# Performance work log

Measured on AMD Instinct MI355X. Metric: run time of the kernel, lower is better.

Reference implementation:

```python
import jax, jax.numpy as jnp
import numpy as np
from jax import lax

RATIOS = jnp.array([0.5, 1.0, 2.0], dtype=jnp.float32)
SCALES = jnp.array([8.0, 16.0, 32.0], dtype=jnp.float32)
IOU_THR = 0.5
BATCH_SIZE = 32            # module-level constant in the source
POS_RATIO = 1.0 / 3.0      # positive_ratio in the source


def _generate_anchors(fh, fw, ih, iw):
    """Vectorized version of RPN.generate_anchors. Returns (A,4) x1y1x2y2 anchors
    and an (A,) inside-image mask (static shapes; mask replaces boolean filtering)."""
    xs = iw / fw
    ys = ih / fh
    xc = (jnp.arange(fw, dtype=jnp.float32) + 0.5) * xs
    yc = (jnp.arange(fh, dtype=jnp.float32) + 0.5) * ys
    gx, gy = jnp.meshgrid(xc, yc, indexing='ij')
    centers = jnp.stack([gx.ravel(), gy.ravel()], axis=1)          # (fh*fw, 2)
    h = jnp.sqrt(SCALES[None, :] ** 2 / RATIOS[:, None]) * ys       # (3,3)
    w = h * RATIOS[:, None] * xs / ys
    wh = jnp.stack([w.ravel(), h.ravel()], axis=1)                  # (9, 2)
    lo = centers[:, None, :] - wh[None, :, :] / 2
    hi = centers[:, None, :] + wh[None, :, :] / 2
    anchors = jnp.concatenate([lo, hi], axis=2).reshape(-1, 4)      # (A, 4)
    inside = ((anchors[:, 0] >= 0) & (anchors[:, 1] >= 0) &
              (anchors[:, 2] <= iw) & (anchors[:, 3] <= ih))
    return anchors, inside


def _iou_matrix(anchors, gts):
    """Pairwise IoU between (A,4) and (G,4) corner boxes -> (A,G). Vectorizes the
    nested python loop in the original."""
    x1 = jnp.maximum(anchors[:, None, 0], gts[None, :, 0])
    y1 = jnp.maximum(anchors[:, None, 1], gts[None, :, 1])
    x2 = jnp.minimum(anchors[:, None, 2], gts[None, :, 2])
    y2 = jnp.minimum(anchors[:, None, 3], gts[None, :, 3])
    inter = jnp.maximum(x2 - x1, 0.0) * jnp.maximum(y2 - y1, 0.0)
    area_a = (anchors[:, 2] - anchors[:, 0]) * (anchors[:, 3] - anchors[:, 1])
    area_g = (gts[:, 2] - gts[:, 0]) * (gts[:, 3] - gts[:, 1])
    union = area_a[:, None] + area_g[None, :] - inter
    return jnp.where(inter > 0, inter / union, 0.0)


def _conv(x, w, b):
    return lax.conv_general_dilated(x, w, (1, 1), 'SAME',
                                    dimension_numbers=('NHWC', 'HWIO', 'NHWC')) + b


def setup_inputs() -> dict:
    key = jax.random.key(0)
    ks = jax.random.split(key, 11)
    B, H, W, C = 8, 64, 64, 512
    IMG = 1024
    std = 0.05  # keras RandomNormal default stddev
    features = jax.random.normal(ks[0], (B, H, W, C), jnp.float32)
    # 8 rows of boxes; rows 2..7 are the object boxes used by the RPN (x1,y1,x2,y2)
    xy = jax.random.uniform(ks[1], (8, 2), jnp.float32) * (IMG * 0.7)
    wh = jax.random.uniform(ks[2], (8, 2), jnp.float32) * (IMG * 0.2) + 16.0
    ground_truths = jnp.concatenate([xy, xy + wh], axis=1)
    return {
        'features': features,
        'ground_truths': ground_truths,
        'conv1_w': jax.random.normal(ks[3], (3, 3, C, 512), jnp.float32) * std,
        'conv1_b': jnp.zeros((512,), jnp.float32),
        'reg_w': jax.random.normal(ks[4], (1, 1, 512, 72), jnp.float32) * std,
        'reg_b': jnp.zeros((72,), jnp.float32),
        'cls_w': jax.random.normal(ks[5], (1, 1, 512, 9), jnp.float32) * std,
        'cls_b': jnp.zeros((9,), jnp.float32),
        'lmk_w': jax.random.normal(ks[6], (1, 1, 512, 54), jnp.float32) * std,
        'lmk_b': jnp.zeros((54,), jnp.float32),
        'img_h': IMG,
        'img_w': IMG,
    }


def reference(features, ground_truths, conv1_w, conv1_b, reg_w, reg_b,
              cls_w, cls_b, lmk_w, lmk_b, img_h, img_w):
    B, H, W, C = features.shape
    anchors, inside = _generate_anchors(H, W, float(img_h), float(img_w))
    A = anchors.shape[0]
    gts = ground_truths[2:]                                   # (6,4)
    ious = _iou_matrix(anchors, gts)                          # (A,6)
    ious = jnp.where(inside[:, None], ious, -1.0)             # outside anchors never match

    best_iou = ious.max(axis=1)
    best_idx = ious.argmax(axis=1)
    gt_best = ious.max(axis=0)
    is_best = ((ious == gt_best[None, :]) & (gt_best[None, :] > -1.0)).any(axis=1)
    labels = jnp.where((best_iou >= IOU_THR) | is_best, 1, 0)
    labels = jnp.where(inside, labels, -1)

    # balanced subsampling (np.random.choice in the original -> rank-of-random trick)
    num_pos = int(POS_RATIO * BATCH_SIZE)
    num_neg = BATCH_SIZE - num_pos
    r = jax.random.uniform(jax.random.key(42), (A,), jnp.float32)

    def keep(mask, n):
        kv = jnp.where(mask, r, jnp.inf)
        order = jnp.argsort(kv)
        rank = jnp.zeros(A, jnp.int32).at[order].set(jnp.arange(A, dtype=jnp.int32))
        return mask & (rank < n)

    pos = keep(labels == 1, num_pos)
    neg = keep(labels == 0, num_neg)
    labels = jnp.where(pos, 1, jnp.where(neg, 0, -1)).astype(jnp.float32)

    eps = jnp.finfo(jnp.float32).eps
    wa = jnp.maximum(anchors[:, 2] - anchors[:, 0], eps)
    ha = jnp.maximum(anchors[:, 3] - anchors[:, 1], eps)
    xa = anchors[:, 0] + wa / 2
    ya = anchors[:, 1] + ha / 2
    mg = gts[best_idx]                                        # (A,4) matched gt
    wg = mg[:, 2] - mg[:, 0]
    hg = mg[:, 3] - mg[:, 1]
    xg = mg[:, 0] + wg / 2
    yg = mg[:, 1] + hg / 2
    deltas = jnp.stack([(xg - xa) / wa, (yg - ya) / ha,
                        jnp.log(wg / wa), jnp.log(hg / ha)], axis=1)
    offsets = jnp.where(pos[:, None], deltas, 0.0)            # (A,4)

    # conv heads on backbone features
    x = jax.nn.relu(_conv(features, conv1_w, conv1_b))
    anchor_deltas = _conv(x, reg_w, reg_b)                    # (B,H,W,72)
    scores = jax.nn.sigmoid(_conv(x, cls_w, cls_b))           # (B,H,W,9)
    landmarks = _conv(x, lmk_w, lmk_b)                        # (B,H,W,54)
    return anchor_deltas, scores, landmarks, labels, offsets
```

## Files before the change

kernel.cpp:

```cpp
#include <hip/hip_runtime.h>
#include <cstdint>
#include <cstddef>


#define A_TOT 36864

typedef unsigned short ushortT;
typedef __attribute__((ext_vector_type(8))) short short8;
typedef __attribute__((ext_vector_type(4))) float f32x4;

typedef __attribute__((address_space(1))) unsigned char gbyte_t;
typedef __attribute__((address_space(3))) unsigned char lbyte_t;

__device__ __forceinline__ void gld_lds16(const void* g, void* l) {
  __builtin_amdgcn_global_load_lds((gbyte_t*)g, (lbyte_t*)l, 16, 0, 0);
}

__device__ __forceinline__ uint32_t rotl32(uint32_t v, int d) { return (v << d) | (v >> (32 - d)); }

__device__ __forceinline__ ushortT f2bf(float f) {
  uint32_t u = __float_as_uint(f);
  uint32_t r = (u + 0x7FFFu + ((u >> 16) & 1u)) >> 16;
  return (ushortT)r;
}

__device__ __forceinline__ uint32_t f2mono(float f) {
  uint32_t b = __float_as_uint(f);
  return b ^ ((b >> 31) ? 0xFFFFFFFFu : 0x80000000u);
}
__device__ __forceinline__ float mono2f(uint32_t u) {
  uint32_t b = (u >> 31) ? (u ^ 0x80000000u) : ~u;
  return __uint_as_float(b);
}

__device__ uint32_t threefry_bits_for(uint32_t a) {
  uint32_t x0 = 0u, x1 = a;
  const uint32_t k0 = 0u, k1 = 42u;
  const uint32_t k2 = k0 ^ k1 ^ 0x1BD11BDAu;
  x0 += k0; x1 += k1;
#define TF_RND(r) { x0 += x1; x1 = rotl32(x1, (r)); x1 ^= x0; }
  TF_RND(13) TF_RND(15) TF_RND(26) TF_RND(6)
  x0 += k1; x1 += k2 + 1u;
  TF_RND(17) TF_RND(29) TF_RND(16) TF_RND(24)
  x0 += k2; x1 += k0 + 2u;
  TF_RND(13) TF_RND(15) TF_RND(26) TF_RND(6)
  x0 += k0; x1 += k1 + 3u;
  TF_RND(17) TF_RND(29) TF_RND(16) TF_RND(24)
  x0 += k1; x1 += k2 + 4u;
  TF_RND(13) TF_RND(15) TF_RND(26) TF_RND(6)
  x0 += k2; x1 += k0 + 5u;
#undef TF_RND
  return x0 ^ x1;
}

struct Anc { float x1, y1, x2, y2; bool inside; };

__device__ __forceinline__ Anc anchor_at(int a, float iw, float ih) {
  Anc A;
  {
    #pragma clang fp contract(off)
    int p = a / 9;
    int q = a - p * 9;
    int i = p >> 6;
    int j = p & 63;
    int ri = q / 3;
    int si = q - ri * 3;
    const float ratios[3] = {0.5f, 1.0f, 2.0f};
    const float scales[3] = {8.0f, 16.0f, 32.0f};
    float xs = iw / 64.0f;
    float ys = ih / 64.0f;
    float cx = ((float)i + 0.5f) * xs;
    float cy = ((float)j + 0.5f) * ys;
    float r = ratios[ri], s = scales[si];
    float h = sqrtf((s * s) / r) * ys;
    float w = h * r * xs / ys;
    A.x1 = cx - w * 0.5f;
    A.y1 = cy - h * 0.5f;
    A.x2 = cx + w * 0.5f;
    A.y2 = cy + h * 0.5f;
    A.inside = (A.x1 >= 0.0f) && (A.y1 >= 0.0f) && (A.x2 <= iw) && (A.y2 <= ih);
  }
  return A;
}

__device__ __forceinline__ float iou_one(const Anc& A, const float* g) {
  #pragma clang fp contract(off)
  float x1 = fmaxf(A.x1, g[0]);
  float y1 = fmaxf(A.y1, g[1]);
  float x2 = fminf(A.x2, g[2]);
  float y2 = fminf(A.y2, g[3]);
  float inter = fmaxf(x2 - x1, 0.0f) * fmaxf(y2 - y1, 0.0f);
  float area_a = (A.x2 - A.x1) * (A.y2 - A.y1);
  float area_g = (g[2] - g[0]) * (g[3] - g[1]);
  float un = (area_a + area_g) - inter;
  return inter > 0.0f ? (inter / un) : 0.0f;
}

__global__ __launch_bounds__(256) void labels_gtmax_kernel(
    const float* __restrict__ gtr, const int* __restrict__ pih, const int* __restrict__ piw,
    uint32_t* __restrict__ gtbest_bits) {
  __shared__ float s_gt[6][4];
  __shared__ float s_red[4][6];
  int tid = threadIdx.x;
  if (tid < 24) ((float*)s_gt)[tid] = gtr[8 + tid];
  __syncthreads();
  float iw = (float)piw[0], ih = (float)pih[0];
  int a = blockIdx.x * 256 + tid;
  Anc A = anchor_at(a, iw, ih);
  int w = tid >> 6;
  #pragma unroll
  for (int g = 0; g < 6; ++g) {
    float v = A.inside ? iou_one(A, s_gt[g]) : -1.0f;
    for (int off = 32; off > 0; off >>= 1) v = fmaxf(v, __shfl_down(v, off, 64));
    if ((tid & 63) == 0) s_red[w][g] = v;
  }
  __syncthreads();
  if (tid < 6) {
    float m = fmaxf(fmaxf(s_red[0][tid], s_red[1][tid]), fmaxf(s_red[2][tid], s_red[3][tid]));
    atomicMax(&gtbest_bits[tid], f2mono(m));
  }
}

__global__ __launch_bounds__(256) void labels_code_kernel(
    const float* __restrict__ gtr, const int* __restrict__ pih, const int* __restrict__ piw,
    const uint32_t* __restrict__ gtbest_bits, uint32_t* __restrict__ L) {
  __shared__ float s_gt[6][4];
  __shared__ float s_gb[6];
  int tid = threadIdx.x;
  if (tid < 24) ((float*)s_gt)[tid] = gtr[8 + tid];
  if (tid < 6) s_gb[tid] = mono2f(gtbest_bits[tid]);
  __syncthreads();
  float iw = (float)piw[0], ih = (float)pih[0];
  int a = blockIdx.x * 256 + tid;
  Anc A = anchor_at(a, iw, ih);
  uint32_t code;
  if (!A.inside) {
    code = 2u;
  } else {
    float best = -1.0f;
    bool isb = false;
    #pragma unroll
    for (int g = 0; g < 6; ++g) {
      float v = iou_one(A, s_gt[g]);
      best = fmaxf(best, v);
      if (v == s_gb[g] && s_gb[g] > -1.0f) isb = true;
    }
    code = (best >= 0.5f || isb) ? 1u : 0u;
  }
  uint32_t m = threefry_bits_for((uint32_t)a) >> 9;
  L[a] = (m << 2) | code;
}

__global__ __launch_bounds__(1024) void labels_select_kernel(
    const uint32_t* __restrict__ L, unsigned long long* __restrict__ Tsel) {
  __shared__ int hist[2][512];
  __shared__ unsigned long long list[2][512];
  __shared__ int lcnt[2];
  __shared__ int s_b[2], s_r[2];
  int tid = threadIdx.x;
  hist[tid >> 9][tid & 511] = 0;
  if (tid < 2) lcnt[tid] = 0;
  __syncthreads();
  for (int a = tid; a < A_TOT; a += 1024) {
    uint32_t v = L[a];
    uint32_t c = v & 3u;
    if (c < 2u) atomicAdd(&hist[c][v >> 16], 1);
  }
  __syncthreads();
  if (tid < 2) {
    int need = (tid == 1) ? 10 : 22;
    int tot = 0;
    for (int i = 0; i < 512; ++i) tot += hist[tid][i];
    int b = -1, r = 0, cum = 0;
    if (tot > need) {
      for (int i = 0; i < 512; ++i) {
        if (cum + hist[tid][i] >= need) { b = i; r = need - cum; break; }
        cum += hist[tid][i];
      }
    }
    s_b[tid] = b; s_r[tid] = r;
    if (b < 0) Tsel[tid] = ~0ull;
  }
  __syncthreads();
  for (int a = tid; a < A_TOT; a += 1024) {
    uint32_t v = L[a];
    uint32_t c = v & 3u;
    if (c < 2u && s_b[c] == (int)(v >> 16)) {
      int idx = atomicAdd(&lcnt[c], 1);
      if (idx < 512) list[c][idx] = (((unsigned long long)(v >> 2)) << 16) | (unsigned)a;
    }
  }
  __syncthreads();
  #pragma unroll
  for (int c = 0; c < 2; ++c) {
    if (s_b[c] < 0) continue;
    int n = lcnt[c] < 512 ? lcnt[c] : 512;
    if (tid < n) {
      unsigned long long k = list[c][tid];
      int rank = 1;
      for (int i = 0; i < n; ++i) rank += (list[c][i] < k) ? 1 : 0;
      if (rank == s_r[c]) Tsel[c] = k;
    }
  }
}

__global__ __launch_bounds__(256) void labels_final_kernel(
    const uint32_t* __restrict__ L, const unsigned long long* __restrict__ Tsel,
    const float* __restrict__ gtr, const int* __restrict__ pih, const int* __restrict__ piw,
    float* __restrict__ labels_out, float* __restrict__ offs_out) {
  __shared__ float s_gt[6][4];
  int tid = threadIdx.x;
  if (tid < 24) ((float*)s_gt)[tid] = gtr[8 + tid];
  __syncthreads();
  float iw = (float)piw[0], ih = (float)pih[0];
  int a = blockIdx.x * 256 + tid;
  uint32_t v = L[a];
  uint32_t code = v & 3u;
  unsigned long long K = (((unsigned long long)(v >> 2)) << 16) | (unsigned)a;
  bool pos = (code == 1u) && (K <= Tsel[1]);
  bool neg = (code == 0u) && (K <= Tsel[0]);
  labels_out[a] = pos ? 1.0f : (neg ? 0.0f : -1.0f);
  float o0 = 0.0f, o1 = 0.0f, o2 = 0.0f, o3 = 0.0f;
  if (pos) {
    #pragma clang fp contract(off)
    Anc A = anchor_at(a, iw, ih);
    int bi = 0;
    float bv = iou_one(A, s_gt[0]);
    for (int g = 1; g < 6; ++g) {
      float vg = iou_one(A, s_gt[g]);
      if (vg > bv) { bv = vg; bi = g; }
    }
    const float eps = 1.1920928955078125e-07f;
    float wa = fmaxf(A.x2 - A.x1, eps);
    float ha = fmaxf(A.y2 - A.y1, eps);
    float xa = A.x1 + wa * 0.5f;
    float ya = A.y1 + ha * 0.5f;
    const float* g = s_gt[bi];
    float wg = g[2] - g[0];
    float hg = g[3] - g[1];
    float xg = g[0] + wg * 0.5f;
    float yg = g[1] + hg * 0.5f;
    o0 = (xg - xa) / wa;
    o1 = (yg - ya) / ha;
    o2 = logf(wg / wa);
    o3 = logf(hg / ha);
  }
  offs_out[a * 4 + 0] = o0;
  offs_out[a * 4 + 1] = o1;
  offs_out[a * 4 + 2] = o2;
  offs_out[a * 4 + 3] = o3;
}

__global__ __launch_bounds__(256) void prep_wt_kernel(
    const float* __restrict__ w, ushortT* __restrict__ Wt) {
  __shared__ float tile[64][65];
  int blk = blockIdx.x;
  int kk = blk / 64;
  int rem = blk - kk * 64;
  int ic0 = (rem >> 3) * 64;
  int oc0 = (rem & 7) * 64;
  int t = threadIdx.x;
  int tr = t >> 6;
  int tc = t & 63;
  #pragma unroll
  for (int r = 0; r < 16; ++r) {
    int ic = tr * 16 + r;
    tile[ic][tc] = w[((size_t)(kk * 512 + ic0 + ic)) * 512 + oc0 + tc];
  }
  __syncthreads();
  #pragma unroll
  for (int r = 0; r < 16; ++r) {
    int oc = tr * 16 + r;
    Wt[((size_t)(kk * 512 + oc0 + oc)) * 512 + ic0 + tc] = f2bf(tile[tc][oc]);
  }
}

__global__ void prep_misc_kernel(const float* __restrict__ feat,
                                 const float* __restrict__ reg_w, const float* __restrict__ cls_w,
                                 const float* __restrict__ lmk_w, const float* __restrict__ reg_b,
                                 const float* __restrict__ cls_b, const float* __restrict__ lmk_b,
                                 ushortT* __restrict__ featbf, ushortT* __restrict__ zrow,
                                 ushortT* __restrict__ Wh, float* __restrict__ bias_all,
                                 uint32_t* __restrict__ gtbest_bits, int do_feat) {
  int idx = blockIdx.x * 256 + threadIdx.x;
  if (do_feat) {
    const float4 f0 = *(const float4*)(feat + (size_t)idx * 8);
    const float4 f1 = *(const float4*)(feat + (size_t)idx * 8 + 4);
    short8 o;
    o[0] = (short)f2bf(f0.x); o[1] = (short)f2bf(f0.y);
    o[2] = (short)f2bf(f0.z); o[3] = (short)f2bf(f0.w);
    o[4] = (short)f2bf(f1.x); o[5] = (short)f2bf(f1.y);
    o[6] = (short)f2bf(f1.z); o[7] = (short)f2bf(f1.w);
    *(short8*)(featbf + (size_t)idx * 8) = o;
  }
  if (idx < 73728) {
    int c = idx >> 9, ic = idx & 511;
    float v = 0.0f;
    if (c < 72) v = reg_w[ic * 72 + c];
    else if (c < 81) v = cls_w[ic * 9 + (c - 72)];
    else if (c < 135) v = lmk_w[ic * 54 + (c - 81)];
    Wh[idx] = f2bf(v);
  }
  if (do_feat && idx < 4096) {
    *(short8*)(zrow + (size_t)idx * 8) = (short8){0, 0, 0, 0, 0, 0, 0, 0};
  }
  if (idx < 144) {
    float bv = 0.0f;
    if (idx < 72) bv = reg_b[idx];
    else if (idx < 81) bv = cls_b[idx - 72];
    else if (idx < 135) bv = lmk_b[idx - 81];
    bias_all[idx] = bv;
  }
  if (idx < 6) gtbest_bits[idx] = f2mono(-1.0f);
}

__global__ __launch_bounds__(256) void conv3x3_mfma_kernel(
    const ushortT* __restrict__ featbf, const ushortT* __restrict__ zrow,
    const ushortT* __restrict__ Wt, const float* __restrict__ bias,
    ushortT* __restrict__ xbf) {
  __shared__ __align__(16) char smem[2][36864];
  const int tid = threadIdx.x;
  const int lane = tid & 63;
  const int w = tid >> 6;
  const int kgrp = lane >> 4;
  const int ln15 = lane & 15;
  const int wm = (w >> 1) * 64;
  const int wn = (w & 1) * 64;
  const int wn16 = wn >> 4;
  const int rowsel = wm >> 6;

  const int lin = blockIdx.x + 4 * blockIdx.y;
  const int swz = (lin & 7) * 128 + (lin >> 3);
  const int j = swz & 127;
  const int xcd = swz >> 7;
  const int oc0 = (j >> 5) * 128;
  const int mb = xcd * 32 + (j & 31);
  const int b = mb >> 5;
  const int y0 = (mb & 31) * 2;

  const int bn15 = lane & 15;
  const int bic = ((lane >> 4) & 3) * 8;

  f32x4 acc[4][4];
  #pragma unroll
  for (int i = 0; i < 4; ++i)
    #pragma unroll
    for (int j2 = 0; j2 < 4; ++j2) acc[i][j2] = (f32x4){0.f, 0.f, 0.f, 0.f};
  const short8 zv = (short8){0, 0, 0, 0, 0, 0, 0, 0};

  auto stageA = [&](int t, int bsel) {
    int ic0 = (t / 3) * 32;
    int dy = (t % 3) - 1;
    char* Ab = smem[bsel];
    #pragma unroll
    for (int i = 0; i < 2; ++i) {
      int c = w + i * 4;
      int h = c >> 2, q = c & 3;
      int ysrc = y0 + h + dy;
      bool vy = (unsigned)ysrc < 64u;
      const ushortT* rowbase = vy ? (featbf + ((size_t)((b * 64 + ysrc) * 64)) * 512) : zrow;
      const ushortT* src = rowbase + (size_t)(q * 16 + bn15) * 512 + ic0 + bic;
      gld_lds16(src, Ab + h * 6144 + 1024 + q * 1024);
    }
  };
  auto issueB = [&](int t, int bsel) {
    int ic0 = (t / 3) * 32;
    int ky = t % 3;
    char* Bb = smem[bsel] + 12288;
    #pragma unroll
    for (int i = 0; i < 6; ++i) {
      int c = w + i * 4;
      int kxr = c >> 3, cc = c & 7;
      int kk = ky * 3 + kxr;
      int n = cc * 16 + bn15;
      const ushortT* src = Wt + ((size_t)(kk * 512 + oc0 + n)) * 512 + ic0 + bic;
      gld_lds16(src, Bb + kxr * 8192 + cc * 1024);
    }
  };
  auto computeT = [&](int t, int bsel) {
    const char* Ab = smem[bsel] + rowsel * 6144;
    const char* Bb = smem[bsel] + 12288;
    int dy = (t % 3) - 1;
    int rowv = y0 + rowsel + dy;
    if ((unsigned)rowv >= 64u) return;
    #pragma unroll
    for (int kx = 0; kx < 3; ++kx) {
      const int dx = kx - 1;
      short8 bfr[4];
      #pragma unroll
      for (int j2 = 0; j2 < 4; ++j2)
        bfr[j2] = *(const short8*)(Bb + kx * 8192 + (wn16 + j2) * 1024 + kgrp * 256 + ln15 * 16);
      short8 afr[4];
      #pragma unroll
      for (int i = 0; i < 4; ++i) {
        int xp = i * 16 + ln15 + dx + 16;
        afr[i] = *(const short8*)(Ab + (xp >> 4) * 1024 + kgrp * 256 + (xp & 15) * 16);
      }
      #pragma unroll
      for (int i = 0; i < 4; ++i)
        #pragma unroll
        for (int j2 = 0; j2 < 4; ++j2)
          acc[i][j2] = __builtin_amdgcn_mfma_f32_16x16x32_bf16(afr[i], bfr[j2], acc[i][j2], 0, 0, 0);
    }
  };

  {
    int pc = tid >> 6;
    int h = pc >> 1, side = pc & 1;
    int off = h * 6144 + side * 5120 + (tid & 63) * 16;
    *(short8*)(smem[0] + off) = zv;
    *(short8*)(smem[1] + off) = zv;
  }
  stageA(0, 0);
  issueB(0, 0);
  __syncthreads();

  int buf = 0;
  for (int t = 0; t < 48; ++t) {
    if (t < 47) { stageA(t + 1, buf ^ 1); issueB(t + 1, buf ^ 1); }
    computeT(t, buf);
    __syncthreads();
    buf ^= 1;
  }

  #pragma unroll
  for (int j2 = 0; j2 < 4; ++j2) {
    int n = oc0 + wn + j2 * 16 + ln15;
    float bv = bias[n];
    #pragma unroll
    for (int i = 0; i < 4; ++i) {
      int mrow = mb * 128 + wm + i * 16 + kgrp * 4;
      #pragma unroll
      for (int r = 0; r < 4; ++r) {
        float v = fmaxf(acc[i][j2][r] + bv, 0.0f);
        xbf[(size_t)(mrow + r) * 512 + n] = f2bf(v);
      }
    }
  }
}

__global__ __launch_bounds__(256) void conv3x3_mfma_fb_kernel(
    const float* __restrict__ feat, const ushortT* __restrict__ Wt,
    const float* __restrict__ bias, ushortT* __restrict__ xbf) {
  __shared__ __align__(16) char smem[2][32768];
  const int tid = threadIdx.x;
  const int lane = tid & 63;
  const int w = tid >> 6;
  const int kgrp = lane >> 4;
  const int ln15 = lane & 15;
  const int wm = (w >> 1) * 64;
  const int wn = (w & 1) * 64;
  const int wn16 = wn >> 4;
  const int lin = blockIdx.x + 4 * blockIdx.y;
  const int swz = (lin & 7) * 128 + (lin >> 3);
  const int oc0 = (swz & 3) * 128;
  const int mb = swz >> 2;
  const int b = mb >> 5;
  const int y0 = (mb & 31) * 2;
  const int sp0 = (tid >> 6) * 16 + (tid & 15);
  const int sk0 = ((tid >> 4) & 3) * 8;
  const int bn15 = lane & 15;
  const int bic = ((lane >> 4) & 3) * 8;

  f32x4 acc[4][4];
  #pragma unroll
  for (int i = 0; i < 4; ++i)
    #pragma unroll
    for (int j = 0; j < 4; ++j) acc[i][j] = (f32x4){0.f, 0.f, 0.f, 0.f};
  const short8 zv = (short8){0, 0, 0, 0, 0, 0, 0, 0};

  auto issueA = [&](int t, float4* aL) {
    int ic0 = (t / 3) * 32;
    int dy = (t % 3) - 1;
    #pragma unroll
    for (int h = 0; h < 2; ++h) {
      int p = sp0 + h * 64;
      int ys = y0 + (p >> 6) + dy;
      ys = ys < 0 ? 0 : (ys > 63 ? 63 : ys);
      const float* sp = feat + ((size_t)((b * 64 + ys) * 64 + (p & 63))) * 512 + ic0 + sk0;
      aL[h * 2 + 0] = *(const float4*)sp;
      aL[h * 2 + 1] = *(const float4*)(sp + 4);
    }
  };
  auto issueB = [&](int t, int bsel) {
    int ic0 = (t / 3) * 32;
    int ky = t % 3;
    char* Bb = smem[bsel] + 8192;
    #pragma unroll
    for (int i = 0; i < 6; ++i) {
      int c = w + i * 4;
      int kxr = c >> 3, cc = c & 7;
      int kk = ky * 3 + kxr;
      int n = cc * 16 + bn15;
      const ushortT* src = Wt + ((size_t)(kk * 512 + oc0 + n)) * 512 + ic0 + bic;
      gld_lds16(src, Bb + kxr * 8192 + cc * 1024);
    }
  };
  auto writeA = [&](const float4* aL, int bsel) {
    char* Ab = smem[bsel];
    #pragma unroll
    for (int h = 0; h < 2; ++h) {
      float4 f0 = aL[h * 2 + 0], f1 = aL[h * 2 + 1];
      short8 o;
      o[0] = (short)f2bf(f0.x); o[1] = (short)f2bf(f0.y);
      o[2] = (short)f2bf(f0.z); o[3] = (short)f2bf(f0.w);
      o[4] = (short)f2bf(f1.x); o[5] = (short)f2bf(f1.y);
      o[6] = (short)f2bf(f1.z); o[7] = (short)f2bf(f1.w);
      *(short8*)(Ab + h * 4096 + tid * 16) = o;
    }
  };
  auto computeT = [&](int t, int bsel) {
    const char* Ab = smem[bsel];
    const char* Bb = smem[bsel] + 8192;
    int dy = (t % 3) - 1;
    int rowv = y0 + (wm >> 6) + dy;
    if ((unsigned)rowv >= 64u) return;
    #pragma unroll
    for (int kx = 0; kx < 3; ++kx) {
      const int dx = kx - 1;
      short8 bfr[4];
      #pragma unroll
      for (int j = 0; j < 4; ++j)
        bfr[j] = *(const short8*)(Bb + kx * 8192 + (wn16 + j) * 1024 + kgrp * 256 + ln15 * 16);
      short8 afr[4];
      #pragma unroll
      for (int i = 0; i < 4; ++i) {
        int xin = i * 16 + ln15 + dx;
        bool ok = (unsigned)xin < 64u;
        int p_in = wm + (ok ? xin : 0);
        short8 v = *(const short8*)(Ab + (p_in >> 4) * 1024 + kgrp * 256 + (p_in & 15) * 16);
        afr[i] = ok ? v : zv;
      }
      #pragma unroll
      for (int i = 0; i < 4; ++i)
        #pragma unroll
        for (int j = 0; j < 4; ++j)
          acc[i][j] = __builtin_amdgcn_mfma_f32_16x16x32_bf16(afr[i], bfr[j], acc[i][j], 0, 0, 0);
    }
  };

  {
    float4 aL[4];
    issueA(0, aL);
    issueB(0, 0);
    writeA(aL, 0);
  }
  __syncthreads();

  int buf = 0;
  for (int t = 0; t < 48; ++t) {
    float4 aN[4];
    if (t < 47) { issueA(t + 1, aN); issueB(t + 1, buf ^ 1); }
    computeT(t, buf);
    if (t < 47) writeA(aN, buf ^ 1);
    __syncthreads();
    buf ^= 1;
  }

  #pragma unroll
  for (int j = 0; j < 4; ++j) {
    int n = oc0 + wn + j * 16 + ln15;
    float bv = bias[n];
    #pragma unroll
    for (int i = 0; i < 4; ++i) {
      int mrow = mb * 128 + wm + i * 16 + kgrp * 4;
      #pragma unroll
      for (int r = 0; r < 4; ++r) {
        float v = fmaxf(acc[i][j][r] + bv, 0.0f);
        xbf[(size_t)(mrow + r) * 512 + n] = f2bf(v);
      }
    }
  }
}

__global__ __launch_bounds__(256) void heads_mfma_kernel(
    const ushortT* __restrict__ x, const ushortT* __restrict__ Wh,
    const float* __restrict__ bias_all,
    float* __restrict__ out_deltas, float* __restrict__ out_scores, float* __restrict__ out_lmk) {
  __shared__ __align__(16) char smem[2][17408];
  const int tid = threadIdx.x;
  const int lane = tid & 63;
  const int w = tid >> 6;
  const int kgrp = lane >> 4;
  const int ln15 = lane & 15;
  const int lin = blockIdx.x;
  const int swz = (lin & 7) * 32 + (lin >> 3);
  const int m0 = swz * 128;
  const int bn15 = lane & 15;
  const int bic = ((lane >> 4) & 3) * 8;

  f32x4 acc[2][9];
  #pragma unroll
  for (int i = 0; i < 2; ++i)
    #pragma unroll
    for (int j = 0; j < 9; ++j) acc[i][j] = (f32x4){0.f, 0.f, 0.f, 0.f};

  auto stage = [&](int t, int bsel) {
    int k0 = t * 32;
    char* Ab = smem[bsel];
    char* Bb = smem[bsel] + 8192;
    #pragma unroll
    for (int i = 0; i < 2; ++i) {
      int cc = w + i * 4;
      int p = cc * 16 + bn15;
      gld_lds16(x + ((size_t)(m0 + p)) * 512 + k0 + bic, Ab + cc * 1024);
    }
    for (int c = w; c < 9; c += 4) {
      int n = c * 16 + bn15;
      gld_lds16(Wh + ((size_t)n) * 512 + k0 + bic, Bb + c * 1024);
    }
  };
  auto computeH = [&](int bsel) {
    const char* Ab = smem[bsel];
    const char* Bb = smem[bsel] + 8192;
    short8 afr[2], bfr[9];
    #pragma unroll
    for (int i = 0; i < 2; ++i)
      afr[i] = *(const short8*)(Ab + (w * 2 + i) * 1024 + kgrp * 256 + ln15 * 16);
    #pragma unroll
    for (int j = 0; j < 9; ++j)
      bfr[j] = *(const short8*)(Bb + j * 1024 + kgrp * 256 + ln15 * 16);
    #pragma unroll
    for (int i = 0; i < 2; ++i)
      #pragma unroll
      for (int j = 0; j < 9; ++j)
        acc[i][j] = __builtin_amdgcn_mfma_f32_16x16x32_bf16(afr[i], bfr[j], acc[i][j], 0, 0, 0);
  };

  stage(0, 0);
  __syncthreads();
  int buf = 0;
  for (int t = 0; t < 16; ++t) {
    if (t < 15) stage(t + 1, buf ^ 1);
    computeH(buf);
    __syncthreads();
    buf ^= 1;
  }

  #pragma unroll
  for (int j = 0; j < 9; ++j) {
    int c = j * 16 + ln15;
    float bv = bias_all[c];
    #pragma unroll
    for (int i = 0; i < 2; ++i) {
      int mrow = m0 + w * 32 + i * 16 + kgrp * 4;
      #pragma unroll
      for (int r = 0; r < 4; ++r) {
        size_t m = (size_t)(mrow + r);
        float v = acc[i][j][r] + bv;
        if (c < 72) out_deltas[m * 72 + c] = v;
        else if (c < 81) out_scores[m * 9 + (c - 72)] = 1.0f / (1.0f + expf(-v));
        else if (c < 135) out_lmk[m * 54 + (c - 81)] = v;
      }
    }
  }
}

extern "C" void kernel_launch(void* const* d_in, const int* in_sizes, int n_in,
                              void* d_out, int out_size, void* d_ws, size_t ws_size,
                              hipStream_t stream) {
  const float* feat    = (const float*)d_in[0];
  const float* gtr     = (const float*)d_in[1];
  const float* conv1_w = (const float*)d_in[2];
  const float* conv1_b = (const float*)d_in[3];
  const float* reg_w   = (const float*)d_in[4];
  const float* reg_b   = (const float*)d_in[5];
  const float* cls_w   = (const float*)d_in[6];
  const float* cls_b   = (const float*)d_in[7];
  const float* lmk_w   = (const float*)d_in[8];
  const float* lmk_b   = (const float*)d_in[9];
  const int*   pih     = (const int*)d_in[10];
  const int*   piw     = (const int*)d_in[11];

  float* out = (float*)d_out;
  float* deltas = out;
  float* scores = out + 2359296;
  float* lmk    = out + 2654208;
  float* labels = out + 4423680;
  float* offs   = out + 4460544;

  ushortT*  Wt          = (ushortT*)d_ws;
  ushortT*  Wh          = (ushortT*)((char*)d_ws + 4718592);
  float*    bias_all    = (float*)((char*)d_ws + 4866048);
  uint32_t* gtbest_bits = (uint32_t*)((char*)d_ws + 4866688);
  unsigned long long* Tsel = (unsigned long long*)((char*)d_ws + 4866752);
  ushortT*  xbf         = (ushortT*)((char*)d_ws + 4866816);
  uint32_t* L           = (uint32_t*)((char*)d_ws + 38421248);
  ushortT*  featbf      = (ushortT*)((char*)d_ws + 38568704);
  ushortT*  zrow        = (ushortT*)((char*)d_ws + 72123136);

  const bool use_bf16A = ws_size >= 72188672ull;

  prep_wt_kernel<<<576, 256, 0, stream>>>(conv1_w, Wt);
  prep_misc_kernel<<<8192, 256, 0, stream>>>(feat, reg_w, cls_w, lmk_w,
                                             reg_b, cls_b, lmk_b, featbf, zrow,
                                             Wh, bias_all, gtbest_bits,
                                             use_bf16A ? 1 : 0);

  dim3 gconv(4, 256);
  if (use_bf16A) {
    conv3x3_mfma_kernel<<<gconv, 256, 0, stream>>>(featbf, zrow, Wt, conv1_b, xbf);
  } else {
    conv3x3_mfma_fb_kernel<<<gconv, 256, 0, stream>>>(feat, Wt, conv1_b, xbf);
  }

  heads_mfma_kernel<<<256, 256, 0, stream>>>(xbf, Wh, bias_all, deltas, scores, lmk);

  labels_gtmax_kernel<<<144, 256, 0, stream>>>(gtr, pih, piw, gtbest_bits);
  labels_code_kernel<<<144, 256, 0, stream>>>(gtr, pih, piw, gtbest_bits, L);
  labels_select_kernel<<<1, 1024, 0, stream>>>(L, Tsel);
  labels_final_kernel<<<144, 256, 0, stream>>>(L, Tsel, gtr, pih, piw, labels, offs);
}
```

Measured before the change: 257.9 us.

## Enlarge conv3x3 MFMA tile to 256x128 per block with per-wave rows

Each conv block now covers 4 image rows (256 pixels) by 128 output channels instead of 2 rows by 128. Each wave owns one full row and all 8 N sub-tiles, so every weight tile loaded into LDS is reused across twice as many pixels. Horizontal padding now comes from masking the A fragments in registers rather than from zeroed LDS halo columns, and the grid is halved. In exchange each wave holds twice as many accumulators (128 floats), which raises register pressure and may lower occupancy despite the launch_bounds hint of 2. The old per-row early exit for out-of-image rows is gone, so those rows are handled as zero loads instead.

```diff
diff --git a/kernel.cpp b/kernel.cpp
--- a/kernel.cpp
+++ b/kernel.cpp
@@ -314,59 +314,56 @@
   if (idx < 6) gtbest_bits[idx] = f2mono(-1.0f);
 }
 
-__global__ __launch_bounds__(256) void conv3x3_mfma_kernel(
+__global__ __launch_bounds__(256, 2) void conv3x3_mfma_kernel(
     const ushortT* __restrict__ featbf, const ushortT* __restrict__ zrow,
     const ushortT* __restrict__ Wt, const float* __restrict__ bias,
     ushortT* __restrict__ xbf) {
-  __shared__ __align__(16) char smem[2][36864];
+  __shared__ __align__(16) char Asm[2][16384];
+  __shared__ __align__(16) char Bsm[2][24576];
   const int tid = threadIdx.x;
   const int lane = tid & 63;
   const int w = tid >> 6;
   const int kgrp = lane >> 4;
   const int ln15 = lane & 15;
-  const int wm = (w >> 1) * 64;
-  const int wn = (w & 1) * 64;
-  const int wn16 = wn >> 4;
-  const int rowsel = wm >> 6;
-
-  const int lin = blockIdx.x + 4 * blockIdx.y;
-  const int swz = (lin & 7) * 128 + (lin >> 3);
-  const int j = swz & 127;
-  const int xcd = swz >> 7;
-  const int oc0 = (j >> 5) * 128;
-  const int mb = xcd * 32 + (j & 31);
-  const int b = mb >> 5;
-  const int y0 = (mb & 31) * 2;
+
+  const int lin = blockIdx.x + 2 * blockIdx.y;
+  const int swz = (lin & 7) * 64 + (lin >> 3);
+  const int j = swz & 63;
+  const int xcd = swz >> 6;
+  const int oc0 = (j >> 4) * 128;
+  const int mt = xcd * 16 + (j & 15);
+  const int b = mt >> 4;
+  const int y0 = (mt & 15) * 4;
 
   const int bn15 = lane & 15;
   const int bic = ((lane >> 4) & 3) * 8;
 
-  f32x4 acc[4][4];
+  f32x4 acc[4][8];
   #pragma unroll
   for (int i = 0; i < 4; ++i)
     #pragma unroll
-    for (int j2 = 0; j2 < 4; ++j2) acc[i][j2] = (f32x4){0.f, 0.f, 0.f, 0.f};
+    for (int j2 = 0; j2 < 8; ++j2) acc[i][j2] = (f32x4){0.f, 0.f, 0.f, 0.f};
   const short8 zv = (short8){0, 0, 0, 0, 0, 0, 0, 0};
 
   auto stageA = [&](int t, int bsel) {
     int ic0 = (t / 3) * 32;
     int dy = (t % 3) - 1;
-    char* Ab = smem[bsel];
-    #pragma unroll
-    for (int i = 0; i < 2; ++i) {
+    char* Ab = Asm[bsel];
+    #pragma unroll
+    for (int i = 0; i < 4; ++i) {
       int c = w + i * 4;
-      int h = c >> 2, q = c & 3;
-      int ysrc = y0 + h + dy;
+      int s = c >> 2, q = c & 3;
+      int ysrc = y0 + s + dy;
       bool vy = (unsigned)ysrc < 64u;
       const ushortT* rowbase = vy ? (featbf + ((size_t)((b * 64 + ysrc) * 64)) * 512) : zrow;
       const ushortT* src = rowbase + (size_t)(q * 16 + bn15) * 512 + ic0 + bic;
-      gld_lds16(src, Ab + h * 6144 + 1024 + q * 1024);
+      gld_lds16(src, Ab + s * 4096 + q * 1024);
     }
   };
   auto issueB = [&](int t, int bsel) {
     int ic0 = (t / 3) * 32;
     int ky = t % 3;
-    char* Bb = smem[bsel] + 12288;
+    char* Bb = Bsm[bsel];
     #pragma unroll
     for (int i = 0; i < 6; ++i) {
       int c = w + i * 4;
@@ -377,40 +374,33 @@
       gld_lds16(src, Bb + kxr * 8192 + cc * 1024);
     }
   };
-  auto computeT = [&](int t, int bsel) {
-    const char* Ab = smem[bsel] + rowsel * 6144;
-    const char* Bb = smem[bsel] + 12288;
-    int dy = (t % 3) - 1;
-    int rowv = y0 + rowsel + dy;
-    if ((unsigned)rowv >= 64u) return;
+  auto computeT = [&](int bsel) {
+    const char* Ab = Asm[bsel] + w * 4096;
+    const char* Bb = Bsm[bsel];
     #pragma unroll
     for (int kx = 0; kx < 3; ++kx) {
       const int dx = kx - 1;
-      short8 bfr[4];
-      #pragma unroll
-      for (int j2 = 0; j2 < 4; ++j2)
-        bfr[j2] = *(const short8*)(Bb + kx * 8192 + (wn16 + j2) * 1024 + kgrp * 256 + ln15 * 16);
+      short8 bfr[8];
+      #pragma unroll
+      for (int j2 = 0; j2 < 8; ++j2)
+        bfr[j2] = *(const short8*)(Bb + kx * 8192 + j2 * 1024 + kgrp * 256 + ln15 * 16);
       short8 afr[4];
       #pragma unroll
       for (int i = 0; i < 4; ++i) {
-        int xp = i * 16 + ln15 + dx + 16;
-        afr[i] = *(const short8*)(Ab + (xp >> 4) * 1024 + kgrp * 256 + (xp & 15) * 16);
+        int xin = i * 16 + ln15 + dx;
+        bool ok = (unsigned)xin < 64u;
+        int p = ok ? xin : 0;
+        short8 v = *(const short8*)(Ab + (p >> 4) * 1024 + kgrp * 256 + (p & 15) * 16);
+        afr[i] = ok ? v : zv;
       }
       #pragma unroll
       for (int i = 0; i < 4; ++i)
         #pragma unroll
-        for (int j2 = 0; j2 < 4; ++j2)
+        for (int j2 = 0; j2 < 8; ++j2)
           acc[i][j2] = __builtin_amdgcn_mfma_f32_16x16x32_bf16(afr[i], bfr[j2], acc[i][j2], 0, 0, 0);
     }
   };
 
-  {
-    int pc = tid >> 6;
-    int h = pc >> 1, side = pc & 1;
-    int off = h * 6144 + side * 5120 + (tid & 63) * 16;
-    *(short8*)(smem[0] + off) = zv;
-    *(short8*)(smem[1] + off) = zv;
-  }
   stageA(0, 0);
   issueB(0, 0);
   __syncthreads();
@@ -418,18 +408,18 @@
   int buf = 0;
   for (int t = 0; t < 48; ++t) {
     if (t < 47) { stageA(t + 1, buf ^ 1); issueB(t + 1, buf ^ 1); }
-    computeT(t, buf);
+    computeT(buf);
     __syncthreads();
     buf ^= 1;
   }
 
   #pragma unroll
-  for (int j2 = 0; j2 < 4; ++j2) {
-    int n = oc0 + wn + j2 * 16 + ln15;
+  for (int j2 = 0; j2 < 8; ++j2) {
+    int n = oc0 + j2 * 16 + ln15;
     float bv = bias[n];
     #pragma unroll
     for (int i = 0; i < 4; ++i) {
-      int mrow = mb * 128 + wm + i * 16 + kgrp * 4;
+      int mrow = mt * 256 + w * 64 + i * 16 + kgrp * 4;
       #pragma unroll
       for (int r = 0; r < 4; ++r) {
         float v = fmaxf(acc[i][j2][r] + bv, 0.0f);
@@ -697,10 +687,11 @@
                                              Wh, bias_all, gtbest_bits,
                                              use_bf16A ? 1 : 0);
 
-  dim3 gconv(4, 256);
   if (use_bf16A) {
+    dim3 gconv(2, 256);
     conv3x3_mfma_kernel<<<gconv, 256, 0, stream>>>(featbf, zrow, Wt, conv1_b, xbf);
   } else {
+    dim3 gconv(4, 256);
     conv3x3_mfma_fb_kernel<<<gconv, 256, 0, stream>>>(feat, Wt, conv1_b, xbf);
   }
 
```

New measurement: 222.0 us (median of 2 runs). 13.9% less time.
